# Optimization experiments

Hardware: AMD Instinct MI355X
Metric: run time of the kernel (lower is better)

Reference implementation:

```python
import jax, jax.numpy as jnp
import numpy as np

N, B, OBS, ACT, E = 8, 8192, 128, 32, 128  # num_agents, batch, obs, act, embedding_dim


def setup_inputs() -> dict:
    key = jax.random.key(0)
    ks = jax.random.split(key, 14)
    rn = lambda k, shape: jax.random.normal(k, shape, dtype=jnp.float32) * 0.05
    return {
        'obs': jax.random.normal(ks[0], (N, B, OBS), dtype=jnp.float32),
        'act': jax.random.normal(ks[1], (N, B, ACT), dtype=jnp.float32),
        'Wg': rn(ks[2], (N, OBS + ACT, E)), 'bg': rn(ks[3], (N, E)),
        'Wq': rn(ks[4], (N, E, E)), 'bq': rn(ks[5], (N, E)),
        'Wk': rn(ks[6], (N, E, E)), 'bk': rn(ks[7], (N, E)),
        'Wv': rn(ks[8], (N, E, E)), 'bv': rn(ks[9], (N, E)),
        'W1': rn(ks[10], (N, (N + 1) * E, E)), 'b1': rn(ks[11], (N, E)),
        'W2': rn(ks[12], (N, E, 1)), 'b2': rn(ks[13], (N, 1)),
    }


def reference(obs, act, Wg, bg, Wq, bq, Wk, bk, Wv, bv, W1, b1, W2, b2):
    # per-agent embeddings e_i = relu(g_i([obs_i; act_i]))           [N,B,E]
    oa = jnp.concatenate([obs, act], axis=-1)
    e = jax.nn.relu(jnp.einsum('nbd,nde->nbe', oa, Wg) + bg[:, None, :])

    # per-(agent i, head l) queries and per-(agent j, head l) keys   [N,L,B,E]
    q = jnp.einsum('ibe,lef->ilbf', e, Wq) + bq[None, :, None, :]
    k = jnp.einsum('jbe,lef->jlbf', e, Wk) + bk[None, :, None, :]

    # scalar per-sample score key.dot(query); original applies softmax to this
    # single scalar, which is identically 1 -> softmax over a singleton axis.
    scores = jnp.einsum('ilbe,jlbe->iljb', q, k)          # [N,L,N,B]
    alpha = jax.nn.softmax(scores[..., None], axis=-1)[..., 0]  # == ones

    # values v_{l,j} = leaky_relu(V_l(e_j))                          [L,N,B,E]
    v = jax.nn.leaky_relu(jnp.einsum('jbe,lef->ljbf', e, Wv) + bv[:, None, None, :])

    # exclude j == i, aggregate: total_{i,l} = sum_{j!=i} alpha * v_{l,j}
    mask = (1.0 - jnp.eye(N, dtype=e.dtype))              # [i,j]
    w = alpha * mask[:, None, :, None]                    # [N,L,N,B]
    total = jnp.einsum('iljb,ljbe->ilbe', w, v)           # [N,L,B,E]

    # x_i = concat over heads l -> [N,B,L*E]
    xi = jnp.transpose(total, (0, 2, 1, 3)).reshape(N, B, N * E)

    # q_i = f_i([x_i; e_i])
    h = jnp.concatenate([xi, e], axis=-1)                 # [N,B,(N+1)E]
    h = jax.nn.relu(jnp.einsum('nbd,nde->nbe', h, W1) + b1[:, None, :])
    out = jnp.einsum('nbe,neo->nbo', h, W2) + b2[:, None, :]  # [N,B,1]
    return out
```

## Files before the change

kernel.cpp:

```cpp
#include <hip/hip_runtime.h>

#define DEV static __device__ __forceinline__

typedef __attribute__((ext_vector_type(8))) short short8;
typedef __attribute__((ext_vector_type(8))) __bf16 bf16x8;
typedef __attribute__((ext_vector_type(4))) float f32x4;


DEV short f2bf(float f) { return __builtin_bit_cast(short, (__bf16)f); }
DEV float bf2f(short h) {
  unsigned u = ((unsigned)(unsigned short)h) << 16;
  return __builtin_bit_cast(float, u);
}
DEV f32x4 mfma16(short8 a, short8 b, f32x4 c) {
  return __builtin_amdgcn_mfma_f32_16x16x32_bf16(
      __builtin_bit_cast(bf16x8, a), __builtin_bit_cast(bf16x8, b), c, 0, 0, 0);
}
DEV void async_copy16(short* lds, const short* g) {
  __builtin_amdgcn_global_load_lds(
      (const __attribute__((address_space(1))) void*)g,
      (__attribute__((address_space(3))) void*)lds, 16, 0, 0);
}

template <int GPC, int SRC_STRIDE, int LDS_STRIDE>
DEV void stage_bt(short* lds, const short* src, int tid) {
  constexpr int TOTAL = 128 * GPC;
  #pragma unroll
  for (int g0 = 0; g0 < TOTAL; g0 += 256) {
    int g = g0 + tid;
    int c = g / GPC, kg = g % GPC;
    *(short8*)(lds + c * LDS_STRIDE + kg * 8) =
        *(const short8*)(src + c * SRC_STRIDE + kg * 8);
  }
}

__global__ __launch_bounds__(256) void k0_tr(const float* __restrict__ Wg,
                                             const float* __restrict__ Wv,
                                             const float* __restrict__ W1,
                                             short* __restrict__ WgT,
                                             short* __restrict__ WvP,
                                             short* __restrict__ W1P) {
  int g = blockIdx.x * 256 + threadIdx.x;
  short8 o;
  if (g < 20480) {
    int n = g / 2560, rem = g % 2560;
    int c = rem & 127, kg = rem >> 7;
    const float* src = Wg + n * 20480;
    #pragma unroll
    for (int j = 0; j < 8; ++j) o[j] = f2bf(src[(size_t)(kg * 8 + j) * 128 + c]);
    *(short8*)(WgT + n * 20480 + c * 160 + kg * 8) = o;
  } else if (g < 36864) {
    int g2 = g - 20480;
    int n = g2 >> 11, rem = g2 & 2047;
    int c = rem & 127, kg = rem >> 7;
    const float* src = Wv + n * 16384;
    #pragma unroll
    for (int j = 0; j < 8; ++j) o[j] = f2bf(src[(size_t)(16 * j + kg) * 128 + c]);
    *(short8*)(WvP + n * 16384 + c * 128 + kg * 8) = o;
  } else {
    int g3 = g - 36864;
    int n = g3 / 18432, rem = g3 % 18432;
    int c = rem & 127, kg = rem >> 7;
    int chunk = kg >> 4, kl = kg & 15;
    const float* src = W1 + (size_t)n * 147456;
    #pragma unroll
    for (int j = 0; j < 8; ++j)
      o[j] = f2bf(src[(size_t)(chunk * 128 + 16 * j + kl) * 128 + c]);
    *(short8*)(W1P + (size_t)n * 147456 + c * 1152 + kg * 8) = o;
  }
}

__global__ __launch_bounds__(256) void k1_e(const float* __restrict__ obs,
                                            const float* __restrict__ act,
                                            const short* __restrict__ WgT,
                                            const float* __restrict__ bg,
                                            short* __restrict__ eB) {
  __shared__ __align__(16) short BW[128 * 168];
  const int btile = blockIdx.x, n = blockIdx.y, tid = threadIdx.x;
  stage_bt<20, 160, 168>(BW, WgT + n * 20480, tid);
  __syncthreads();
  const int lane = tid & 63, wave = tid >> 6, lr = lane & 15, kg = lane >> 4;
  const int rowbase = btile * 64 + wave * 16;
  f32x4 acc[8];
  #pragma unroll
  for (int m = 0; m < 8; ++m) acc[m] = f32x4{0.f, 0.f, 0.f, 0.f};
  const float* obsp = obs + (size_t)(n * 8192 + rowbase + lr) * 128;
  const float* actp = act + (size_t)(n * 8192 + rowbase + lr) * 32;
  #pragma unroll
  for (int ks = 0; ks < 5; ++ks) {
    const float* ap = (ks < 4) ? (obsp + ks * 32 + kg * 8) : (actp + kg * 8);
    float4 p0 = *(const float4*)ap;
    float4 p1 = *(const float4*)(ap + 4);
    short8 a;
    a[0] = f2bf(p0.x); a[1] = f2bf(p0.y); a[2] = f2bf(p0.z); a[3] = f2bf(p0.w);
    a[4] = f2bf(p1.x); a[5] = f2bf(p1.y); a[6] = f2bf(p1.z); a[7] = f2bf(p1.w);
    #pragma unroll
    for (int m = 0; m < 8; ++m) {
      short8 b = *(const short8*)(&BW[(m * 16 + lr) * 168 + ks * 32 + kg * 8]);
      acc[m] = mfma16(a, b, acc[m]);
    }
  }
  float bgv[8];
  #pragma unroll
  for (int m = 0; m < 8; ++m) bgv[m] = bg[n * 128 + m * 16 + lr];
  #pragma unroll
  for (int r = 0; r < 4; ++r) {
    short8 pkt;
    #pragma unroll
    for (int m = 0; m < 8; ++m) {
      float x = acc[m][r] + bgv[m];
      pkt[m] = f2bf(x > 0.f ? x : 0.f);
    }
    *(short8*)(eB + (size_t)(n * 8192 + rowbase + kg * 4 + r) * 128 + lr * 8) = pkt;
  }
}

__global__ __launch_bounds__(256) void k2_A(const short* __restrict__ eB,
                                            const short* __restrict__ WvP,
                                            const float* __restrict__ bv,
                                            short* __restrict__ AB) {
  __shared__ __align__(16) short BW[128 * 136];
  const int btile = blockIdx.x, l = blockIdx.y, tid = threadIdx.x;
  stage_bt<16, 128, 136>(BW, WvP + l * 16384, tid);
  __syncthreads();
  const int lane = tid & 63, wave = tid >> 6, lr = lane & 15, kg = lane >> 4;
  const int rowbase = btile * 64 + wave * 16;
  float bvv[8];
  #pragma unroll
  for (int m = 0; m < 8; ++m) bvv[m] = bv[l * 128 + m * 16 + lr];
  f32x4 Sacc[8];
  #pragma unroll
  for (int m = 0; m < 8; ++m) Sacc[m] = f32x4{0.f, 0.f, 0.f, 0.f};
  for (int j = 0; j < 8; ++j) {
    f32x4 acc[8];
    #pragma unroll
    for (int m = 0; m < 8; ++m) acc[m] = f32x4{0.f, 0.f, 0.f, 0.f};
    const short* ep = eB + (size_t)(j * 8192 + rowbase + lr) * 128;
    #pragma unroll
    for (int ks = 0; ks < 4; ++ks) {
      short8 a = *(const short8*)(ep + ks * 32 + kg * 8);
      #pragma unroll
      for (int m = 0; m < 8; ++m) {
        short8 b = *(const short8*)(&BW[(m * 16 + lr) * 136 + ks * 32 + kg * 8]);
        acc[m] = mfma16(a, b, acc[m]);
      }
    }
    #pragma unroll
    for (int m = 0; m < 8; ++m)
      #pragma unroll
      for (int r = 0; r < 4; ++r) {
        float x = acc[m][r] + bvv[m];
        Sacc[m][r] += (x > 0.f ? x : 0.01f * x);
      }
  }
  for (int j = 0; j < 8; ++j) {
    f32x4 acc[8];
    #pragma unroll
    for (int m = 0; m < 8; ++m) acc[m] = f32x4{0.f, 0.f, 0.f, 0.f};
    const short* ep = eB + (size_t)(j * 8192 + rowbase + lr) * 128;
    #pragma unroll
    for (int ks = 0; ks < 4; ++ks) {
      short8 a = *(const short8*)(ep + ks * 32 + kg * 8);
      #pragma unroll
      for (int m = 0; m < 8; ++m) {
        short8 b = *(const short8*)(&BW[(m * 16 + lr) * 136 + ks * 32 + kg * 8]);
        acc[m] = mfma16(a, b, acc[m]);
      }
    }
    #pragma unroll
    for (int r = 0; r < 4; ++r) {
      short8 pkt;
      #pragma unroll
      for (int m = 0; m < 8; ++m) {
        float x = acc[m][r] + bvv[m];
        x = (x > 0.f) ? x : 0.01f * x;
        pkt[m] = f2bf(Sacc[m][r] - x);
      }
      *(short8*)(AB + (size_t)(j * 8192 + rowbase + kg * 4 + r) * 1024 +
                 l * 128 + lr * 8) = pkt;
    }
  }
}

__global__ __launch_bounds__(512, 2) void k3_g(const short* __restrict__ eB,
                                               const short* __restrict__ AB,
                                               const short* __restrict__ W1P,
                                               const float* __restrict__ b1,
                                               const float* __restrict__ W2,
                                               const float* __restrict__ b2,
                                               float* __restrict__ out) {
  __shared__ __align__(16) short BW[2][128 * 128];
  const int bid = blockIdx.x;
  const int i = bid & 7;
  const int btile = bid >> 3;
  const int tid = threadIdx.x;
  const int lane = tid & 63, wave = tid >> 6, lr = lane & 15, kg = lane >> 4;
  const int lr8 = lane & 7;
  const int rowbase = btile * 128 + wave * 16;
  const short* w1 = W1P + (size_t)i * 147456;

#define STAGE_W1(buf, koff)                                                    \
  {                                                                            \
    _Pragma("unroll") for (int t = 0; t < 4; ++t) {                            \
      int G = t * 512 + tid;                                                   \
      int cG = G >> 4, gl = G & 15;                                            \
      async_copy16((buf) + (t * 512 + wave * 64) * 8,                          \
                   w1 + cG * 1152 + (koff) + ((gl ^ (cG & 7)) << 3));          \
    }                                                                          \
  }

  const short* abase = AB + (size_t)(i * 8192 + rowbase + lr) * 1024;
  const short* ebase = eB + (size_t)(i * 8192 + rowbase + lr) * 128;

  short8 ea[4], aa[4], aap[4];
  #pragma unroll
  for (int ks = 0; ks < 4; ++ks) {
    ea[ks] = *(const short8*)(ebase + (ks * 4 + kg) * 8);
    aa[ks] = *(const short8*)(abase + (ks * 4 + kg) * 8);
  }
  f32x4 hacc[8];
  #pragma unroll
  for (int m = 0; m < 8; ++m) hacc[m] = f32x4{0.f, 0.f, 0.f, 0.f};

  STAGE_W1(BW[0], 0);
  for (int c = 0; c < 9; ++c) {
    __syncthreads();
    if (c < 8) { STAGE_W1(BW[(c + 1) & 1], (c + 1 == 8) ? 1024 : (c + 1) * 128); }
    if (c + 1 < 8) {
      #pragma unroll
      for (int ks = 0; ks < 4; ++ks)
        aap[ks] = *(const short8*)(abase + (c + 1) * 128 + (ks * 4 + kg) * 8);
    }
    const short* bw = BW[c & 1];
    #pragma unroll
    for (int ks = 0; ks < 4; ++ks)
      #pragma unroll
      for (int m = 0; m < 8; ++m) {
        short8 b = *(const short8*)(bw + (m * 16 + lr) * 128 +
                                    (((ks * 4 + kg) ^ lr8) << 3));
        hacc[m] = mfma16(aa[ks], b, hacc[m]);
      }
    if (c + 1 < 8) {
      #pragma unroll
      for (int ks = 0; ks < 4; ++ks) aa[ks] = aap[ks];
    } else {
      #pragma unroll
      for (int ks = 0; ks < 4; ++ks) aa[ks] = ea[ks];
    }
  }
#undef STAGE_W1

  float sacc[4] = {0.f, 0.f, 0.f, 0.f};
  #pragma unroll
  for (int m = 0; m < 8; ++m) {
    int col = m * 16 + lr;
    float b1v = b1[i * 128 + col];
    float w2v = W2[i * 128 + col];
    #pragma unroll
    for (int r = 0; r < 4; ++r) {
      float h = hacc[m][r] + b1v;
      h = h > 0.f ? h : 0.f;
      sacc[r] += h * w2v;
    }
  }
  #pragma unroll
  for (int r = 0; r < 4; ++r) {
    float v = sacc[r];
    v += __shfl_xor(v, 1);
    v += __shfl_xor(v, 2);
    v += __shfl_xor(v, 4);
    v += __shfl_xor(v, 8);
    if (lr == 0) out[i * 8192 + rowbase + kg * 4 + r] = v + b2[i];
  }
}

extern "C" void kernel_launch(void* const* d_in, const int* in_sizes, int n_in,
                              void* d_out, int out_size, void* d_ws, size_t ws_size,
                              hipStream_t stream) {
  const float* obs = (const float*)d_in[0];
  const float* act = (const float*)d_in[1];
  const float* Wg  = (const float*)d_in[2];
  const float* bg  = (const float*)d_in[3];
  const float* Wv  = (const float*)d_in[8];
  const float* bv  = (const float*)d_in[9];
  const float* W1  = (const float*)d_in[10];
  const float* b1  = (const float*)d_in[11];
  const float* W2  = (const float*)d_in[12];
  const float* b2  = (const float*)d_in[13];
  float* out = (float*)d_out;

  short* eB  = (short*)d_ws;
  short* AB  = eB + (size_t)8 * 8192 * 128;
  short* WgT = AB + (size_t)8 * 8192 * 1024;
  short* WvP = WgT + 163840;
  short* W1P = WvP + 131072;

  k0_tr<<<720, 256, 0, stream>>>(Wg, Wv, W1, WgT, WvP, W1P);
  k1_e<<<dim3(128, 8), 256, 0, stream>>>(obs, act, WgT, bg, eB);
  k2_A<<<dim3(128, 8), 256, 0, stream>>>(eB, WvP, bv, AB);
  k3_g<<<512, 512, 0, stream>>>(eB, AB, W1P, b1, W2, b2, out);
}
```

Baseline: 112.0 us.

## Store per-head value sums and subtract self term in final GEMM

Result: no change. 109.9 us (-1.8%).

```diff
diff --git a/kernel.cpp b/kernel.cpp
--- a/kernel.cpp
+++ b/kernel.cpp
@@ -20,6 +20,12 @@
   __builtin_amdgcn_global_load_lds(
       (const __attribute__((address_space(1))) void*)g,
       (__attribute__((address_space(3))) void*)lds, 16, 0, 0);
+}
+DEV void nt_store8(short* p, short8 v) {
+  __builtin_nontemporal_store(v, (short8*)p);
+}
+DEV short8 nt_load8(const short* p) {
+  return __builtin_nontemporal_load((const short8*)p);
 }
 
 template <int GPC, int SRC_STRIDE, int LDS_STRIDE>
@@ -112,6 +118,167 @@
       pkt[m] = f2bf(x > 0.f ? x : 0.f);
     }
     *(short8*)(eB + (size_t)(n * 8192 + rowbase + kg * 4 + r) * 128 + lr * 8) = pkt;
+  }
+}
+
+__global__ __launch_bounds__(256) void k2_V(const short* __restrict__ eB,
+                                            const short* __restrict__ WvP,
+                                            const float* __restrict__ bv,
+                                            short* __restrict__ SB,
+                                            short* __restrict__ VBg) {
+  __shared__ __align__(16) short BW[128 * 136];
+  const int btile = blockIdx.x, l = blockIdx.y, tid = threadIdx.x;
+  stage_bt<16, 128, 136>(BW, WvP + l * 16384, tid);
+  __syncthreads();
+  const int lane = tid & 63, wave = tid >> 6, lr = lane & 15, kg = lane >> 4;
+  const int rowbase = btile * 64 + wave * 16;
+  float bvv[8];
+  #pragma unroll
+  for (int m = 0; m < 8; ++m) bvv[m] = bv[l * 128 + m * 16 + lr];
+  f32x4 Sacc[8];
+  #pragma unroll
+  for (int m = 0; m < 8; ++m) Sacc[m] = f32x4{0.f, 0.f, 0.f, 0.f};
+  for (int j = 0; j < 8; ++j) {
+    f32x4 acc[8];
+    #pragma unroll
+    for (int m = 0; m < 8; ++m) acc[m] = f32x4{0.f, 0.f, 0.f, 0.f};
+    const short* ep = eB + (size_t)(j * 8192 + rowbase + lr) * 128;
+    #pragma unroll
+    for (int ks = 0; ks < 4; ++ks) {
+      short8 a = *(const short8*)(ep + ks * 32 + kg * 8);
+      #pragma unroll
+      for (int m = 0; m < 8; ++m) {
+        short8 b = *(const short8*)(&BW[(m * 16 + lr) * 136 + ks * 32 + kg * 8]);
+        acc[m] = mfma16(a, b, acc[m]);
+      }
+    }
+    #pragma unroll
+    for (int r = 0; r < 4; ++r) {
+      short8 pkt;
+      #pragma unroll
+      for (int m = 0; m < 8; ++m) {
+        float x = acc[m][r] + bvv[m];
+        x = (x > 0.f) ? x : 0.01f * x;
+        Sacc[m][r] += x;
+        pkt[m] = f2bf(x);
+      }
+      nt_store8(VBg + (size_t)((j * 8 + l) * 8192 + rowbase + kg * 4 + r) * 128 +
+                    lr * 8,
+                pkt);
+    }
+  }
+  #pragma unroll
+  for (int r = 0; r < 4; ++r) {
+    short8 pkt;
+    #pragma unroll
+    for (int m = 0; m < 8; ++m) pkt[m] = f2bf(Sacc[m][r]);
+    *(short8*)(SB + (size_t)(l * 8192 + rowbase + kg * 4 + r) * 128 + lr * 8) = pkt;
+  }
+}
+
+__global__ __launch_bounds__(512, 2) void k3_h(const short* __restrict__ eB,
+                                               const short* __restrict__ SB,
+                                               const short* __restrict__ VBg,
+                                               const short* __restrict__ W1P,
+                                               const float* __restrict__ b1,
+                                               const float* __restrict__ W2,
+                                               const float* __restrict__ b2,
+                                               float* __restrict__ out) {
+  __shared__ __align__(16) short BW[2][128 * 128];
+  const int bid = blockIdx.x;
+  const int i = bid & 7;
+  const int btile = bid >> 3;
+  const int tid = threadIdx.x;
+  const int lane = tid & 63, wave = tid >> 6, lr = lane & 15, kg = lane >> 4;
+  const int lr8 = lane & 7;
+  const int rowbase = btile * 128 + wave * 16;
+  const short* w1 = W1P + (size_t)i * 147456;
+
+#define STAGE_W1(buf, koff)                                                    \
+  {                                                                            \
+    _Pragma("unroll") for (int t = 0; t < 4; ++t) {                            \
+      int G = t * 512 + tid;                                                   \
+      int cG = G >> 4, gl = G & 15;                                            \
+      async_copy16((buf) + (t * 512 + wave * 64) * 8,                          \
+                   w1 + cG * 1152 + (koff) + ((gl ^ (cG & 7)) << 3));          \
+    }                                                                          \
+  }
+
+  const short* sbase = SB + (size_t)(rowbase + lr) * 128;
+  const short* vbase = VBg + (size_t)((i * 8) * 8192 + rowbase + lr) * 128;
+
+  short8 sv[4], vv[4];
+  #pragma unroll
+  for (int ks = 0; ks < 4; ++ks) {
+    sv[ks] = *(const short8*)(sbase + (ks * 4 + kg) * 8);
+    vv[ks] = nt_load8(vbase + (ks * 4 + kg) * 8);
+  }
+  f32x4 hacc[8];
+  #pragma unroll
+  for (int m = 0; m < 8; ++m) hacc[m] = f32x4{0.f, 0.f, 0.f, 0.f};
+
+  STAGE_W1(BW[0], 0);
+  for (int c = 0; c < 9; ++c) {
+    __syncthreads();
+    if (c < 8) { STAGE_W1(BW[(c + 1) & 1], (c + 1 == 8) ? 1024 : (c + 1) * 128); }
+    short8 aa[4];
+    if (c < 8) {
+      #pragma unroll
+      for (int ks = 0; ks < 4; ++ks)
+        #pragma unroll
+        for (int jj = 0; jj < 8; ++jj)
+          aa[ks][jj] = f2bf(bf2f(sv[ks][jj]) - bf2f(vv[ks][jj]));
+      if (c + 1 < 8) {
+        #pragma unroll
+        for (int ks = 0; ks < 4; ++ks) {
+          sv[ks] = *(const short8*)(sbase + (size_t)(c + 1) * 8192 * 128 +
+                                    (ks * 4 + kg) * 8);
+          vv[ks] = nt_load8(vbase + (size_t)(c + 1) * 8192 * 128 +
+                            (ks * 4 + kg) * 8);
+        }
+      } else {
+        #pragma unroll
+        for (int ks = 0; ks < 4; ++ks)
+          sv[ks] = *(const short8*)(
+              eB + (size_t)(i * 8192 + rowbase + lr) * 128 + (ks * 4 + kg) * 8);
+      }
+    } else {
+      #pragma unroll
+      for (int ks = 0; ks < 4; ++ks) aa[ks] = sv[ks];
+    }
+    const short* bw = BW[c & 1];
+    #pragma unroll
+    for (int ks = 0; ks < 4; ++ks)
+      #pragma unroll
+      for (int m = 0; m < 8; ++m) {
+        short8 b = *(const short8*)(bw + (m * 16 + lr) * 128 +
+                                    (((ks * 4 + kg) ^ lr8) << 3));
+        hacc[m] = mfma16(aa[ks], b, hacc[m]);
+      }
+  }
+#undef STAGE_W1
+
+  float sacc[4] = {0.f, 0.f, 0.f, 0.f};
+  #pragma unroll
+  for (int m = 0; m < 8; ++m) {
+    int col = m * 16 + lr;
+    float b1v = b1[i * 128 + col];
+    float w2v = W2[i * 128 + col];
+    #pragma unroll
+    for (int r = 0; r < 4; ++r) {
+      float h = hacc[m][r] + b1v;
+      h = h > 0.f ? h : 0.f;
+      sacc[r] += h * w2v;
+    }
+  }
+  #pragma unroll
+  for (int r = 0; r < 4; ++r) {
+    float v = sacc[r];
+    v += __shfl_xor(v, 1);
+    v += __shfl_xor(v, 2);
+    v += __shfl_xor(v, 4);
+    v += __shfl_xor(v, 8);
+    if (lr == 0) out[i * 8192 + rowbase + kg * 4 + r] = v + b2[i];
   }
 }
 
@@ -289,14 +456,31 @@
   const float* b2  = (const float*)d_in[13];
   float* out = (float*)d_out;
 
-  short* eB  = (short*)d_ws;
-  short* AB  = eB + (size_t)8 * 8192 * 128;
-  short* WgT = AB + (size_t)8 * 8192 * 1024;
-  short* WvP = WgT + 163840;
-  short* W1P = WvP + 131072;
-
-  k0_tr<<<720, 256, 0, stream>>>(Wg, Wv, W1, WgT, WvP, W1P);
-  k1_e<<<dim3(128, 8), 256, 0, stream>>>(obs, act, WgT, bg, eB);
-  k2_A<<<dim3(128, 8), 256, 0, stream>>>(eB, WvP, bv, AB);
-  k3_g<<<512, 512, 0, stream>>>(eB, AB, W1P, b1, W2, b2, out);
-}
+  const size_t E_N = (size_t)8 * 8192 * 128;
+  const size_t V_N = (size_t)64 * 8192 * 128;
+  const size_t W_N = 163840 + 131072 + 1179648;
+  const size_t NEED_FAST = (E_N + V_N + E_N + W_N) * 2;
+
+  if (ws_size >= NEED_FAST) {
+    short* eB  = (short*)d_ws;
+    short* VBg = eB + E_N;
+    short* SB  = VBg + V_N;
+    short* WgT = SB + E_N;
+    short* WvP = WgT + 163840;
+    short* W1P = WvP + 131072;
+    k0_tr<<<720, 256, 0, stream>>>(Wg, Wv, W1, WgT, WvP, W1P);
+    k1_e<<<dim3(128, 8), 256, 0, stream>>>(obs, act, WgT, bg, eB);
+    k2_V<<<dim3(128, 8), 256, 0, stream>>>(eB, WvP, bv, SB, VBg);
+    k3_h<<<512, 512, 0, stream>>>(eB, SB, VBg, W1P, b1, W2, b2, out);
+  } else {
+    short* eB  = (short*)d_ws;
+    short* AB  = eB + E_N;
+    short* WgT = AB + V_N;
+    short* WvP = WgT + 163840;
+    short* W1P = WvP + 131072;
+    k0_tr<<<720, 256, 0, stream>>>(Wg, Wv, W1, WgT, WvP, W1P);
+    k1_e<<<dim3(128, 8), 256, 0, stream>>>(obs, act, WgT, bg, eB);
+    k2_A<<<dim3(128, 8), 256, 0, stream>>>(eB, WvP, bv, AB);
+    k3_g<<<512, 512, 0, stream>>>(eB, AB, W1P, b1, W2, b2, out);
+  }
+}
```

## Store values as fp8 and sums in bf16, reconstruct leave-one-out inputs in final GEMM

Applied to the files above, without the earlier changes.

After: 110.8 us. No clear change (-1.1%).

```diff
diff --git a/kernel.cpp b/kernel.cpp
--- a/kernel.cpp
+++ b/kernel.cpp
@@ -5,6 +5,7 @@
 typedef __attribute__((ext_vector_type(8))) short short8;
 typedef __attribute__((ext_vector_type(8))) __bf16 bf16x8;
 typedef __attribute__((ext_vector_type(4))) float f32x4;
+typedef __attribute__((ext_vector_type(2))) float f32x2;
 
 
 DEV short f2bf(float f) { return __builtin_bit_cast(short, (__bf16)f); }
@@ -20,6 +21,25 @@
   __builtin_amdgcn_global_load_lds(
       (const __attribute__((address_space(1))) void*)g,
       (__attribute__((address_space(3))) void*)lds, 16, 0, 0);
+}
+
+DEV void c_to_a(short* vb, const short8* pkt, short8* aa, int lr, int kg) {
+  #pragma unroll
+  for (int p = 0; p < 2; ++p) {
+    if ((kg >> 1) == p) {
+      #pragma unroll
+      for (int r = 0; r < 4; ++r) {
+        int rl = (kg & 1) * 4 + r;
+        *(short8*)(vb + rl * 128 + ((lr ^ rl) << 3)) = pkt[r];
+      }
+    }
+    if ((lr >> 3) == p) {
+      int rl = lr & 7;
+      #pragma unroll
+      for (int ks = 0; ks < 4; ++ks)
+        aa[ks] = *(const short8*)(vb + rl * 128 + (((ks * 4 + kg) ^ rl) << 3));
+    }
+  }
 }
 
 template <int GPC, int SRC_STRIDE, int LDS_STRIDE>
@@ -74,13 +94,15 @@
                                             const float* __restrict__ act,
                                             const short* __restrict__ WgT,
                                             const float* __restrict__ bg,
-                                            short* __restrict__ eB) {
+                                            short* __restrict__ eA) {
   __shared__ __align__(16) short BW[128 * 168];
+  __shared__ __align__(16) short VB[4][8 * 128];
   const int btile = blockIdx.x, n = blockIdx.y, tid = threadIdx.x;
   stage_bt<20, 160, 168>(BW, WgT + n * 20480, tid);
   __syncthreads();
   const int lane = tid & 63, wave = tid >> 6, lr = lane & 15, kg = lane >> 4;
   const int rowbase = btile * 64 + wave * 16;
+  const int rowtile = btile * 4 + wave;
   f32x4 acc[8];
   #pragma unroll
   for (int m = 0; m < 8; ++m) acc[m] = f32x4{0.f, 0.f, 0.f, 0.f};
@@ -103,28 +125,34 @@
   float bgv[8];
   #pragma unroll
   for (int m = 0; m < 8; ++m) bgv[m] = bg[n * 128 + m * 16 + lr];
-  #pragma unroll
-  for (int r = 0; r < 4; ++r) {
-    short8 pkt;
+  short8 pkt[4];
+  #pragma unroll
+  for (int r = 0; r < 4; ++r)
     #pragma unroll
     for (int m = 0; m < 8; ++m) {
       float x = acc[m][r] + bgv[m];
-      pkt[m] = f2bf(x > 0.f ? x : 0.f);
-    }
-    *(short8*)(eB + (size_t)(n * 8192 + rowbase + kg * 4 + r) * 128 + lr * 8) = pkt;
-  }
-}
-
-__global__ __launch_bounds__(256) void k2_A(const short* __restrict__ eB,
+      pkt[r][m] = f2bf(x > 0.f ? x : 0.f);
+    }
+  short8 ea[4];
+  c_to_a(VB[wave], pkt, ea, lr, kg);
+  #pragma unroll
+  for (int ks = 0; ks < 4; ++ks)
+    *(short8*)(eA + ((size_t)(n * 512 + rowtile) * 256 + ks * 64 + lane) * 8) =
+        ea[ks];
+}
+
+__global__ __launch_bounds__(256) void k2_V(const short* __restrict__ eA,
                                             const short* __restrict__ WvP,
                                             const float* __restrict__ bv,
-                                            short* __restrict__ AB) {
+                                            short* __restrict__ SBf,
+                                            unsigned char* __restrict__ VBf) {
   __shared__ __align__(16) short BW[128 * 136];
+  __shared__ __align__(16) short VB[4][8 * 128];
   const int btile = blockIdx.x, l = blockIdx.y, tid = threadIdx.x;
   stage_bt<16, 128, 136>(BW, WvP + l * 16384, tid);
   __syncthreads();
   const int lane = tid & 63, wave = tid >> 6, lr = lane & 15, kg = lane >> 4;
-  const int rowbase = btile * 64 + wave * 16;
+  const int rowtile = btile * 4 + wave;
   float bvv[8];
   #pragma unroll
   for (int m = 0; m < 8; ++m) bvv[m] = bv[l * 128 + m * 16 + lr];
@@ -132,121 +160,154 @@
   #pragma unroll
   for (int m = 0; m < 8; ++m) Sacc[m] = f32x4{0.f, 0.f, 0.f, 0.f};
   for (int j = 0; j < 8; ++j) {
+    short8 a[4];
+    #pragma unroll
+    for (int ks = 0; ks < 4; ++ks)
+      a[ks] = *(const short8*)(
+          eA + ((size_t)(j * 512 + rowtile) * 256 + ks * 64 + lane) * 8);
     f32x4 acc[8];
     #pragma unroll
     for (int m = 0; m < 8; ++m) acc[m] = f32x4{0.f, 0.f, 0.f, 0.f};
-    const short* ep = eB + (size_t)(j * 8192 + rowbase + lr) * 128;
-    #pragma unroll
-    for (int ks = 0; ks < 4; ++ks) {
-      short8 a = *(const short8*)(ep + ks * 32 + kg * 8);
+    #pragma unroll
+    for (int ks = 0; ks < 4; ++ks)
       #pragma unroll
       for (int m = 0; m < 8; ++m) {
         short8 b = *(const short8*)(&BW[(m * 16 + lr) * 136 + ks * 32 + kg * 8]);
-        acc[m] = mfma16(a, b, acc[m]);
-      }
-    }
-    #pragma unroll
-    for (int m = 0; m < 8; ++m)
-      #pragma unroll
-      for (int r = 0; r < 4; ++r) {
-        float x = acc[m][r] + bvv[m];
-        Sacc[m][r] += (x > 0.f ? x : 0.01f * x);
-      }
-  }
-  for (int j = 0; j < 8; ++j) {
-    f32x4 acc[8];
-    #pragma unroll
-    for (int m = 0; m < 8; ++m) acc[m] = f32x4{0.f, 0.f, 0.f, 0.f};
-    const short* ep = eB + (size_t)(j * 8192 + rowbase + lr) * 128;
+        acc[m] = mfma16(a[ks], b, acc[m]);
+      }
+    short8 pkt[4];
+    #pragma unroll
+    for (int r = 0; r < 4; ++r)
+      #pragma unroll
+      for (int m = 0; m < 8; ++m) {
+        float t = acc[m][r] + bvv[m];
+        t = (t > 0.f) ? t : 0.01f * t;
+        Sacc[m][r] += t;
+        pkt[r][m] = f2bf(t);
+      }
+    short8 va[4];
+    c_to_a(VB[wave], pkt, va, lr, kg);
     #pragma unroll
     for (int ks = 0; ks < 4; ++ks) {
-      short8 a = *(const short8*)(ep + ks * 32 + kg * 8);
-      #pragma unroll
-      for (int m = 0; m < 8; ++m) {
-        short8 b = *(const short8*)(&BW[(m * 16 + lr) * 136 + ks * 32 + kg * 8]);
-        acc[m] = mfma16(a, b, acc[m]);
-      }
-    }
-    #pragma unroll
-    for (int r = 0; r < 4; ++r) {
-      short8 pkt;
-      #pragma unroll
-      for (int m = 0; m < 8; ++m) {
-        float x = acc[m][r] + bvv[m];
-        x = (x > 0.f) ? x : 0.01f * x;
-        pkt[m] = f2bf(Sacc[m][r] - x);
-      }
-      *(short8*)(AB + (size_t)(j * 8192 + rowbase + kg * 4 + r) * 1024 +
-                 l * 128 + lr * 8) = pkt;
-    }
-  }
-}
-
-__global__ __launch_bounds__(512, 2) void k3_g(const short* __restrict__ eB,
-                                               const short* __restrict__ AB,
+      float x[8];
+      #pragma unroll
+      for (int q = 0; q < 8; ++q) x[q] = bf2f(va[ks][q]);
+      unsigned lo = 0, hi = 0;
+      lo = __builtin_amdgcn_cvt_pk_fp8_f32(x[0], x[1], lo, false);
+      lo = __builtin_amdgcn_cvt_pk_fp8_f32(x[2], x[3], lo, true);
+      hi = __builtin_amdgcn_cvt_pk_fp8_f32(x[4], x[5], hi, false);
+      hi = __builtin_amdgcn_cvt_pk_fp8_f32(x[6], x[7], hi, true);
+      uint2 o{lo, hi};
+      *(uint2*)(VBf + ((size_t)((j * 8 + l) * 512 + rowtile) * 256 + ks * 64 +
+                       lane) * 8) = o;
+    }
+  }
+  short8 pkt[4];
+  #pragma unroll
+  for (int r = 0; r < 4; ++r)
+    #pragma unroll
+    for (int m = 0; m < 8; ++m) pkt[r][m] = f2bf(Sacc[m][r]);
+  short8 sa[4];
+  c_to_a(VB[wave], pkt, sa, lr, kg);
+  #pragma unroll
+  for (int ks = 0; ks < 4; ++ks)
+    *(short8*)(SBf + ((size_t)(l * 512 + rowtile) * 256 + ks * 64 + lane) * 8) =
+        sa[ks];
+}
+
+__global__ __launch_bounds__(256, 4) void k3_h(const short* __restrict__ eA,
+                                               const short* __restrict__ SBf,
+                                               const unsigned char* __restrict__ VBf,
                                                const short* __restrict__ W1P,
                                                const float* __restrict__ b1,
                                                const float* __restrict__ W2,
                                                const float* __restrict__ b2,
                                                float* __restrict__ out) {
-  __shared__ __align__(16) short BW[2][128 * 128];
+  __shared__ __align__(16) short BW[2][128 * 64];
   const int bid = blockIdx.x;
   const int i = bid & 7;
   const int btile = bid >> 3;
   const int tid = threadIdx.x;
   const int lane = tid & 63, wave = tid >> 6, lr = lane & 15, kg = lane >> 4;
   const int lr8 = lane & 7;
-  const int rowbase = btile * 128 + wave * 16;
+  const int rowbase = btile * 64 + wave * 16;
+  const int rowtile = btile * 4 + wave;
   const short* w1 = W1P + (size_t)i * 147456;
 
 #define STAGE_W1(buf, koff)                                                    \
   {                                                                            \
     _Pragma("unroll") for (int t = 0; t < 4; ++t) {                            \
-      int G = t * 512 + tid;                                                   \
-      int cG = G >> 4, gl = G & 15;                                            \
-      async_copy16((buf) + (t * 512 + wave * 64) * 8,                          \
+      int G = t * 256 + tid;                                                   \
+      int cG = G >> 3, gl = G & 7;                                             \
+      async_copy16((buf) + (t * 256 + wave * 64) * 8,                          \
                    w1 + cG * 1152 + (koff) + ((gl ^ (cG & 7)) << 3));          \
     }                                                                          \
   }
 
-  const short* abase = AB + (size_t)(i * 8192 + rowbase + lr) * 1024;
-  const short* ebase = eB + (size_t)(i * 8192 + rowbase + lr) * 128;
-
-  short8 ea[4], aa[4], aap[4];
-  #pragma unroll
-  for (int ks = 0; ks < 4; ++ks) {
-    ea[ks] = *(const short8*)(ebase + (ks * 4 + kg) * 8);
-    aa[ks] = *(const short8*)(abase + (ks * 4 + kg) * 8);
+  short8 sv[2];
+  uint2 vv[2];
+  #pragma unroll
+  for (int ks = 0; ks < 2; ++ks) {
+    sv[ks] = *(const short8*)(
+        SBf + ((size_t)rowtile * 256 + ks * 64 + lane) * 8);
+    vv[ks] = *(const uint2*)(
+        VBf + ((size_t)((i * 8) * 512 + rowtile) * 256 + ks * 64 + lane) * 8);
   }
   f32x4 hacc[8];
   #pragma unroll
   for (int m = 0; m < 8; ++m) hacc[m] = f32x4{0.f, 0.f, 0.f, 0.f};
 
   STAGE_W1(BW[0], 0);
-  for (int c = 0; c < 9; ++c) {
+  for (int c = 0; c < 18; ++c) {
     __syncthreads();
-    if (c < 8) { STAGE_W1(BW[(c + 1) & 1], (c + 1 == 8) ? 1024 : (c + 1) * 128); }
-    if (c + 1 < 8) {
-      #pragma unroll
-      for (int ks = 0; ks < 4; ++ks)
-        aap[ks] = *(const short8*)(abase + (c + 1) * 128 + (ks * 4 + kg) * 8);
+    if (c < 17) { STAGE_W1(BW[(c + 1) & 1], (c + 1) * 64); }
+    short8 aa[2];
+    if (c < 16) {
+      #pragma unroll
+      for (int ks = 0; ks < 2; ++ks) {
+        f32x2 f01 = __builtin_amdgcn_cvt_pk_f32_fp8((int)vv[ks].x, false);
+        f32x2 f23 = __builtin_amdgcn_cvt_pk_f32_fp8((int)vv[ks].x, true);
+        f32x2 f45 = __builtin_amdgcn_cvt_pk_f32_fp8((int)vv[ks].y, false);
+        f32x2 f67 = __builtin_amdgcn_cvt_pk_f32_fp8((int)vv[ks].y, true);
+        aa[ks][0] = f2bf(bf2f(sv[ks][0]) - f01.x);
+        aa[ks][1] = f2bf(bf2f(sv[ks][1]) - f01.y);
+        aa[ks][2] = f2bf(bf2f(sv[ks][2]) - f23.x);
+        aa[ks][3] = f2bf(bf2f(sv[ks][3]) - f23.y);
+        aa[ks][4] = f2bf(bf2f(sv[ks][4]) - f45.x);
+        aa[ks][5] = f2bf(bf2f(sv[ks][5]) - f45.y);
+        aa[ks][6] = f2bf(bf2f(sv[ks][6]) - f67.x);
+        aa[ks][7] = f2bf(bf2f(sv[ks][7]) - f67.y);
+      }
+    } else {
+      aa[0] = sv[0];
+      aa[1] = sv[1];
+    }
+    if (c + 1 < 16) {
+      int l = (c + 1) >> 1, h = (c + 1) & 1;
+      #pragma unroll
+      for (int ks = 0; ks < 2; ++ks) {
+        sv[ks] = *(const short8*)(
+            SBf + (((size_t)l * 512 + rowtile) * 256 + h * 128 + ks * 64 + lane) * 8);
+        vv[ks] = *(const uint2*)(
+            VBf + (((size_t)(i * 8 + l) * 512 + rowtile) * 256 + h * 128 +
+                   ks * 64 + lane) * 8);
+      }
+    } else if (c + 1 < 18) {
+      int h = c + 1 - 16;
+      #pragma unroll
+      for (int ks = 0; ks < 2; ++ks)
+        sv[ks] = *(const short8*)(
+            eA + (((size_t)i * 512 + rowtile) * 256 + h * 128 + ks * 64 + lane) * 8);
     }
     const short* bw = BW[c & 1];
     #pragma unroll
-    for (int ks = 0; ks < 4; ++ks)
+    for (int ks = 0; ks < 2; ++ks)
       #pragma unroll
       for (int m = 0; m < 8; ++m) {
-        short8 b = *(const short8*)(bw + (m * 16 + lr) * 128 +
+        short8 b = *(const short8*)(bw + (m * 16 + lr) * 64 +
                                     (((ks * 4 + kg) ^ lr8) << 3));
         hacc[m] = mfma16(aa[ks], b, hacc[m]);
       }
-    if (c + 1 < 8) {
-      #pragma unroll
-      for (int ks = 0; ks < 4; ++ks) aa[ks] = aap[ks];
-    } else {
-      #pragma unroll
-      for (int ks = 0; ks < 4; ++ks) aa[ks] = ea[ks];
-    }
   }
 #undef STAGE_W1
 
@@ -289,14 +350,18 @@
   const float* b2  = (const float*)d_in[13];
   float* out = (float*)d_out;
 
-  short* eB  = (short*)d_ws;
-  short* AB  = eB + (size_t)8 * 8192 * 128;
-  short* WgT = AB + (size_t)8 * 8192 * 1024;
+  const size_t E_N = (size_t)8 * 8192 * 128;
+  const size_t V_B = (size_t)64 * 8192 * 128;
+
+  short* eA  = (short*)d_ws;
+  unsigned char* VBf = (unsigned char*)(eA + E_N);
+  short* SBf = (short*)(VBf + V_B);
+  short* WgT = SBf + E_N;
   short* WvP = WgT + 163840;
   short* W1P = WvP + 131072;
 
   k0_tr<<<720, 256, 0, stream>>>(Wg, Wv, W1, WgT, WvP, W1P);
-  k1_e<<<dim3(128, 8), 256, 0, stream>>>(obs, act, WgT, bg, eB);
-  k2_A<<<dim3(128, 8), 256, 0, stream>>>(eB, WvP, bv, AB);
-  k3_g<<<512, 512, 0, stream>>>(eB, AB, W1P, b1, W2, b2, out);
-}
+  k1_e<<<dim3(128, 8), 256, 0, stream>>>(obs, act, WgT, bg, eA);
+  k2_V<<<dim3(128, 8), 256, 0, stream>>>(eA, WvP, bv, SBf, VBf);
+  k3_h<<<1024, 256, 0, stream>>>(eA, SBf, VBf, W1P, b1, W2, b2, out);
+}
```
